# Optimization experiments

Hardware: AMD Instinct MI355X
Metric: run time of the kernel (lower is better)

## Reference

```python
import jax, jax.numpy as jnp
import numpy as np
from jax import lax

B, C, L, K = 8, 256, 4096, 65
PAD = K // 2  # torch: int(kernel.shape[-1] / 2) = 32 -> same-length output for odd K


def depthwise_corr(x, k):
    """Depthwise cross-correlation (torch conv1d semantics, no kernel flip).
    x: [B, C, L] float32, k: [K] float32 (same kernel shared by all channels,
    matching kernel.repeat(seq_len, 1)). Returns [B, C, L]."""
    w = jnp.broadcast_to(k.reshape(1, 1, K), (C, 1, K))  # [C, 1, K]
    return lax.conv_general_dilated(
        x, w, window_strides=(1,), padding=[(PAD, PAD)],
        dimension_numbers=("NCH", "OIH", "NCH"), feature_group_count=C)


def setup_inputs() -> dict:
    key = jax.random.key(0)
    k1, k2, k3 = jax.random.split(key, 3)
    return {
        "x": jax.random.normal(k1, (B, C, L), dtype=jnp.float32),
        "kernel_real": jax.random.normal(k2, (K,), dtype=jnp.float32),
        "kernel_imag": jax.random.normal(k3, (K,), dtype=jnp.float32),
        "weights_mag": jnp.ones((1, C, 1), dtype=jnp.float32),
        "weights_angle": jnp.ones((1, C, 1), dtype=jnp.float32),
    }


def reference(x, kernel_real, kernel_imag, weights_mag, weights_angle):
    # mf_coeffs = conj(kernel) -> weight = kernel_real - 1j*kernel_imag.
    # Input x is real (imag=0 after .to(complex64)), so complex conv splits
    # into two real depthwise correlations.
    yr = depthwise_corr(x, kernel_real)            # [B, C, L]
    yi = -depthwise_corr(x, kernel_imag)           # [B, C, L]
    y = lax.complex(yr, yi)                        # complex64 [B, C, L]

    # torch.std over dims (1,2), unbiased (correction=1), complex -> real std
    mean = jnp.mean(y, axis=(1, 2), keepdims=True)
    n = C * L
    var = jnp.sum(jnp.abs(y - mean) ** 2, axis=(1, 2), keepdims=True) / (n - 1)
    y = y / jnp.sqrt(var)                          # real std broadcasts over complex

    # weights_mag * y * exp(-1j * weights_angle)
    phase = lax.complex(jnp.cos(weights_angle), -jnp.sin(weights_angle))  # [1, C, 1]
    y = weights_mag * y * phase

    # FFT over the channel dim (dim=-2), then fftshift on that dim
    return jnp.fft.fftshift(jnp.fft.fft(y, axis=-2), axes=-2)
```

## Files before the change

kernel.cpp:

```cpp
#include <hip/hip_runtime.h>
#include <math.h>

#define NB 8
#define NC 256
#define NL 4096
#define NK 65

__device__ float g_stats[NB * 4];

__global__ void zero_stats_kernel() {
    if (threadIdx.x < NB * 4) g_stats[threadIdx.x] = 0.0f;
}


#define LOAD16(W, off)                                                      \
    {                                                                       \
        const int g0_ = l0 + (off);                                         \
        if (g0_ >= 0 && g0_ + 16 <= NL) {         \
            _Pragma("unroll")                                               \
            for (int q = 0; q < 4; ++q) {                                   \
                const float4 v_ = *(const float4*)(xr + g0_ + 4 * q);       \
                W[4*q+0] = v_.x; W[4*q+1] = v_.y;                           \
                W[4*q+2] = v_.z; W[4*q+3] = v_.w;                           \
            }                                                               \
        } else {                                                            \
            _Pragma("unroll")                                               \
            for (int q = 0; q < 16; ++q) {                                  \
                const int g_ = g0_ + q;                                     \
                W[q] = (g_ >= 0 && g_ < NL) ? xr[g_] : 0.0f;                \
            }                                                               \
        }                                                                   \
    }

#define CHUNK16(Lo, Hi, tb)                                                 \
    {                                                                       \
        _Pragma("unroll")                                                   \
        for (int j2 = 0; j2 < 16; ++j2) {                                   \
            const float kr_ = kre[(tb) + j2];        \
            const float ki_ = kim[(tb) + j2];                               \
            _Pragma("unroll")                                               \
            for (int i = 0; i < 16; ++i) {                                  \
                const int wi_ = i + j2;                                     \
                const float xv_ = (wi_ < 16) ? Lo[wi_] : Hi[wi_ - 16];      \
                sr[i] = fmaf(xv_, kr_, sr[i]);                              \
                si[i] = fmaf(xv_, ki_, si[i]);                              \
            }                                                               \
        }                                                                   \
    }

__global__ __launch_bounds__(256) void fused_conv_fft_kernel(
    const float* __restrict__ x,
    const float* __restrict__ kre,
    const float* __restrict__ kim,
    const float* __restrict__ wmag,
    const float* __restrict__ wang,
    float* __restrict__ out,
    int out_size)
{
    __shared__ __align__(16) float4 lbuf4[NC * 9];
    __shared__ float twr[NC], twi[NC];
    __shared__ float red[12];

    const int t = threadIdx.x;
    const int b = blockIdx.x & 7;
    const int l0 = (blockIdx.x >> 3) << 4;

    {
        float ang = (float)t * 0.024543692606170260f;
        float s, c;
        sincosf(ang, &s, &c);
        twr[t] = c; twi[t] = -s;
    }
    float sw, cw;
    sincosf(wang[t], &sw, &cw);
    const float wm = wmag[t];
    const float wgr =  wm * cw;
    const float wgi = -wm * sw;

    const float* xr = x + (size_t)b * NC * NL + (size_t)t * NL;
    const bool interleaved = (out_size >= 2 * NB * NC * NL);

    float sr[16], si[16];
    #pragma unroll
    for (int i = 0; i < 16; ++i) { sr[i] = 0.0f; si[i] = 0.0f; }

    float A[16], B[16];
    LOAD16(A, -32);
    LOAD16(B, -16);
    CHUNK16(A, B, 0);
    LOAD16(A, 0);
    CHUNK16(B, A, 16);
    LOAD16(B, 16);
    CHUNK16(A, B, 32);
    LOAD16(A, 32);
    CHUNK16(B, A, 48);
    {
        const float kr_ = kre[64];
        const float ki_ = kim[64];
        #pragma unroll
        for (int i = 0; i < 16; ++i) {
            sr[i] = fmaf(A[i], kr_, sr[i]);
            si[i] = fmaf(A[i], ki_, si[i]);
        }
    }

    float tsr = 0.0f, tsi = 0.0f, tsq = 0.0f;
    #pragma unroll
    for (int i = 0; i < 16; ++i) {
        tsr += sr[i];
        tsi -= si[i];
        tsq = fmaf(sr[i], sr[i], tsq);
        tsq = fmaf(si[i], si[i], tsq);
    }

    #pragma unroll
    for (int k = 0; k < 8; ++k) {
        float4 o;
        o.x = sr[2*k]   * wgr + si[2*k]   * wgi;
        o.y = sr[2*k]   * wgi - si[2*k]   * wgr;
        o.z = sr[2*k+1] * wgr + si[2*k+1] * wgi;
        o.w = sr[2*k+1] * wgi - si[2*k+1] * wgr;
        lbuf4[t * 9 + k] = o;
    }
    __syncthreads();

    #pragma unroll
    for (int s = 0; s < 4; ++s) {
        const int shift = 2 * s;
        const int q = 64 >> shift;
        #pragma unroll
        for (int it = 0; it < 2; ++it) {
            int task = it * 256 + t;
            int lpp = task & 7;
            int m = task >> 3;
            int j = m & (q - 1);
            int blk = m >> (6 - shift);
            int base2 = blk << (8 - shift);
            int e = j << shift;

            int ca = base2 + j;
            float4 a0 = lbuf4[ca*9 + lpp];
            float4 a1 = lbuf4[(ca + q)*9 + lpp];
            float4 a2 = lbuf4[(ca + 2*q)*9 + lpp];
            float4 a3 = lbuf4[(ca + 3*q)*9 + lpp];

            float w1r = twr[e],   w1i = twi[e];
            float w2r = twr[2*e], w2i = twi[2*e];
            float w3r = twr[3*e], w3i = twi[3*e];

            float4 b0, b1, b2, b3;
            {
                float t0r = a0.x + a2.x, t0i = a0.y + a2.y;
                float t1r = a0.x - a2.x, t1i = a0.y - a2.y;
                float t2r = a1.x + a3.x, t2i = a1.y + a3.y;
                float t3r = a1.x - a3.x, t3i = a1.y - a3.y;
                b0.x = t0r + t2r;       b0.y = t0i + t2i;
                float b2r = t0r - t2r,  b2i = t0i - t2i;
                float b1r = t1r + t3i,  b1i = t1i - t3r;
                float b3r = t1r - t3i,  b3i = t1i + t3r;
                b1.x = b1r*w1r - b1i*w1i;  b1.y = b1r*w1i + b1i*w1r;
                b2.x = b2r*w2r - b2i*w2i;  b2.y = b2r*w2i + b2i*w2r;
                b3.x = b3r*w3r - b3i*w3i;  b3.y = b3r*w3i + b3i*w3r;
            }
            {
                float t0r = a0.z + a2.z, t0i = a0.w + a2.w;
                float t1r = a0.z - a2.z, t1i = a0.w - a2.w;
                float t2r = a1.z + a3.z, t2i = a1.w + a3.w;
                float t3r = a1.z - a3.z, t3i = a1.w - a3.w;
                b0.z = t0r + t2r;       b0.w = t0i + t2i;
                float b2r = t0r - t2r,  b2i = t0i - t2i;
                float b1r = t1r + t3i,  b1i = t1i - t3r;
                float b3r = t1r - t3i,  b3i = t1i + t3r;
                b1.z = b1r*w1r - b1i*w1i;  b1.w = b1r*w1i + b1i*w1r;
                b2.z = b2r*w2r - b2i*w2i;  b2.w = b2r*w2i + b2i*w2r;
                b3.z = b3r*w3r - b3i*w3i;  b3.w = b3r*w3i + b3i*w3r;
            }
            lbuf4[ca*9 + lpp]         = b0;
            lbuf4[(ca + q)*9 + lpp]   = b1;
            lbuf4[(ca + 2*q)*9 + lpp] = b2;
            lbuf4[(ca + 3*q)*9 + lpp] = b3;
        }
        __syncthreads();
    }

    #pragma unroll
    for (int it = 0; it < 8; ++it) {
        int task = it * 256 + t;
        int lpp = task & 7;
        int pp = task >> 3;
        float4 v = lbuf4[pp*9 + lpp];
        int k = ((pp & 3) << 6) | (((pp >> 2) & 3) << 4)
              | (((pp >> 4) & 3) << 2) | ((pp >> 6) & 3);
        int cout = k ^ 128;
        if (interleaved) {
            size_t fi = 2 * ((size_t)(b * NC + cout) * NL + l0) + 4 * lpp;
            if (fi + 4 <= (size_t)out_size) *(float4*)(out + fi) = v;
        } else {
            size_t fi = (size_t)(b * NC + cout) * NL + l0 + 2 * lpp;
            if (fi + 2 <= (size_t)out_size) {
                float2 o2; o2.x = v.x; o2.y = v.z;
                *(float2*)(out + fi) = o2;
            }
        }
    }

    #pragma unroll
    for (int off = 32; off > 0; off >>= 1) {
        tsr += __shfl_down(tsr, off);
        tsi += __shfl_down(tsi, off);
        tsq += __shfl_down(tsq, off);
    }
    const int lane = t & 63, wv = t >> 6;
    if (lane == 0) { red[wv*3+0] = tsr; red[wv*3+1] = tsi; red[wv*3+2] = tsq; }
    __syncthreads();
    if (t == 0) {
        float a0 = 0.0f, a1 = 0.0f, a2 = 0.0f;
        for (int i = 0; i < 4; ++i) { a0 += red[i*3]; a1 += red[i*3+1]; a2 += red[i*3+2]; }
        atomicAdd(&g_stats[b*4+0], a0);
        atomicAdd(&g_stats[b*4+1], a1);
        atomicAdd(&g_stats[b*4+2], a2);
    }
}

__global__ __launch_bounds__(256) void scale_out_kernel(
    float* __restrict__ out, int out_size)
{
    __shared__ float sinv[NB];
    const int t = threadIdx.x;
    if (t < NB) {
        float sr = g_stats[t*4+0], si = g_stats[t*4+1], sq = g_stats[t*4+2];
        const float n = (float)(NC * NL);
        float var = (sq - (sr*sr + si*si)/n) / (n - 1.0f);
        sinv[t] = rsqrtf(var);
    }
    __syncthreads();

    const int chunk = out_size >> 3;
    const bool p2 = (chunk & (chunk - 1)) == 0;
    const int lb = 31 - __clz(chunk);
    const int n4 = out_size >> 2;
    float4* o4 = (float4*)out;
    for (int i4 = blockIdx.x * blockDim.x + t; i4 < n4;
         i4 += gridDim.x * blockDim.x) {
        int fi = i4 << 2;
        int bidx = p2 ? (fi >> lb) : (fi / chunk);
        float inv = sinv[bidx];
        float4 v = o4[i4];
        v.x *= inv; v.y *= inv; v.z *= inv; v.w *= inv;
        o4[i4] = v;
    }
    int tail0 = n4 << 2;
    int ti = tail0 + blockIdx.x * blockDim.x + t;
    if (ti < out_size) {
        int bidx = p2 ? (ti >> lb) : (ti / chunk);
        out[ti] *= sinv[bidx];
    }
}

extern "C" void kernel_launch(void* const* d_in, const int* in_sizes, int n_in,
                              void* d_out, int out_size, void* d_ws, size_t ws_size,
                              hipStream_t stream)
{
    const float* x   = (const float*)d_in[0];
    const float* kre = (const float*)d_in[1];
    const float* kim = (const float*)d_in[2];
    const float* wm  = (const float*)d_in[3];
    const float* wa  = (const float*)d_in[4];
    float* out = (float*)d_out;
    (void)d_ws; (void)ws_size;

    zero_stats_kernel<<<1, 64, 0, stream>>>();
    fused_conv_fft_kernel<<<NB * (NL / 16), 256, 0, stream>>>(x, kre, kim, wm, wa,
                                                              out, out_size);
    scale_out_kernel<<<2048, 256, 0, stream>>>(out, out_size);
}
```

Measured before the change: 151.6 us.

## Swizzle LDS layout, compute twiddles in registers, replace atomics with per-block partials

The FFT buffer moves from stride-9 padding to an XOR-swizzled layout, which cuts LDS use and allows a launch bound of 5 blocks per CU. Twiddles come from a wave shuffle of one per-lane sincos, with the higher powers derived by complex multiplication rather than read from shared tables. The global atomic statistics and the zeroing kernel are replaced by per-block partial sums that each scale block reduces itself. That block then scales its own contiguous slice, which removes a launch at the cost of redundant reductions across blocks and small twiddle rounding differences.

```diff
diff --git a/kernel.cpp b/kernel.cpp
--- a/kernel.cpp
+++ b/kernel.cpp
@@ -5,13 +5,13 @@
 #define NC 256
 #define NL 4096
 #define NK 65
-
-__device__ float g_stats[NB * 4];
-
-__global__ void zero_stats_kernel() {
-    if (threadIdx.x < NB * 4) g_stats[threadIdx.x] = 0.0f;
-}
-
+#define NSL (NL / 16)
+
+__device__ float4 g_part[NB * NSL];
+
+__device__ __forceinline__ int lidx(int row, int q) {
+    return (row << 3) + (q ^ (row & 7));
+}
 
 #define LOAD16(W, off)                                                      \
     {                                                                       \
@@ -48,7 +48,13 @@
         }                                                                   \
     }
 
-__global__ __launch_bounds__(256) void fused_conv_fft_kernel(
+__device__ __forceinline__ int digitrev_shift(int pp) {
+    int k = ((pp & 3) << 6) | (((pp >> 2) & 3) << 4)
+          | (((pp >> 4) & 3) << 2) | ((pp >> 6) & 3);
+    return k ^ 128;
+}
+
+__global__ __launch_bounds__(256, 5) void fused_conv_fft_kernel(
     const float* __restrict__ x,
     const float* __restrict__ kre,
     const float* __restrict__ kim,
@@ -57,19 +63,20 @@
     float* __restrict__ out,
     int out_size)
 {
-    __shared__ __align__(16) float4 lbuf4[NC * 9];
-    __shared__ float twr[NC], twi[NC];
-    __shared__ float red[12];
+    __shared__ __align__(16) float4 lbuf4[NC * 8];
 
     const int t = threadIdx.x;
     const int b = blockIdx.x & 7;
-    const int l0 = (blockIdx.x >> 3) << 4;
-
+    const int st = blockIdx.x >> 3;
+    const int l0 = st << 4;
+    const int lane = t & 63, wv = t >> 6;
+
+    float tw64r, tw64i;
     {
-        float ang = (float)t * 0.024543692606170260f;
+        float ang = (float)lane * 0.024543692606170260f;
         float s, c;
         sincosf(ang, &s, &c);
-        twr[t] = c; twi[t] = -s;
+        tw64r = c; tw64i = -s;
     }
     float sw, cw;
     sincosf(wang[t], &sw, &cw);
@@ -120,7 +127,7 @@
         o.y = sr[2*k]   * wgi - si[2*k]   * wgr;
         o.z = sr[2*k+1] * wgr + si[2*k+1] * wgi;
         o.w = sr[2*k+1] * wgi - si[2*k+1] * wgr;
-        lbuf4[t * 9 + k] = o;
+        lbuf4[lidx(t, k)] = o;
     }
     __syncthreads();
 
@@ -136,17 +143,25 @@
             int j = m & (q - 1);
             int blk = m >> (6 - shift);
             int base2 = blk << (8 - shift);
-            int e = j << shift;
 
             int ca = base2 + j;
-            float4 a0 = lbuf4[ca*9 + lpp];
-            float4 a1 = lbuf4[(ca + q)*9 + lpp];
-            float4 a2 = lbuf4[(ca + 2*q)*9 + lpp];
-            float4 a3 = lbuf4[(ca + 3*q)*9 + lpp];
-
-            float w1r = twr[e],   w1i = twi[e];
-            float w2r = twr[2*e], w2i = twi[2*e];
-            float w3r = twr[3*e], w3i = twi[3*e];
+            float4 a0 = lbuf4[lidx(ca, lpp)];
+            float4 a1 = lbuf4[lidx(ca + q, lpp)];
+            float4 a2 = lbuf4[lidx(ca + 2*q, lpp)];
+            float4 a3 = lbuf4[lidx(ca + 3*q, lpp)];
+
+            float w1r, w1i;
+            if (s < 3) {
+                int e = j << shift;
+                w1r = __shfl(tw64r, e);
+                w1i = __shfl(tw64i, e);
+            } else {
+                w1r = 1.0f; w1i = 0.0f;
+            }
+            float w2r = fmaf(w1r, w1r, -(w1i * w1i));
+            float w2i = 2.0f * w1r * w1i;
+            float w3r = w2r * w1r - w2i * w1i;
+            float w3i = w2r * w1i + w2i * w1r;
 
             float4 b0, b1, b2, b3;
             {
@@ -175,10 +190,10 @@
                 b2.z = b2r*w2r - b2i*w2i;  b2.w = b2r*w2i + b2i*w2r;
                 b3.z = b3r*w3r - b3i*w3i;  b3.w = b3r*w3i + b3i*w3r;
             }
-            lbuf4[ca*9 + lpp]         = b0;
-            lbuf4[(ca + q)*9 + lpp]   = b1;
-            lbuf4[(ca + 2*q)*9 + lpp] = b2;
-            lbuf4[(ca + 3*q)*9 + lpp] = b3;
+            lbuf4[lidx(ca, lpp)]         = b0;
+            lbuf4[lidx(ca + q, lpp)]     = b1;
+            lbuf4[lidx(ca + 2*q, lpp)]   = b2;
+            lbuf4[lidx(ca + 3*q, lpp)]   = b3;
         }
         __syncthreads();
     }
@@ -188,10 +203,8 @@
         int task = it * 256 + t;
         int lpp = task & 7;
         int pp = task >> 3;
-        float4 v = lbuf4[pp*9 + lpp];
-        int k = ((pp & 3) << 6) | (((pp >> 2) & 3) << 4)
-              | (((pp >> 4) & 3) << 2) | ((pp >> 6) & 3);
-        int cout = k ^ 128;
+        float4 v = lbuf4[lidx(pp, lpp)];
+        int cout = digitrev_shift(pp);
         if (interleaved) {
             size_t fi = 2 * ((size_t)(b * NC + cout) * NL + l0) + 4 * lpp;
             if (fi + 4 <= (size_t)out_size) *(float4*)(out + fi) = v;
@@ -210,50 +223,63 @@
         tsi += __shfl_down(tsi, off);
         tsq += __shfl_down(tsq, off);
     }
-    const int lane = t & 63, wv = t >> 6;
-    if (lane == 0) { red[wv*3+0] = tsr; red[wv*3+1] = tsi; red[wv*3+2] = tsq; }
+    __syncthreads();
+    float* redf = (float*)lbuf4;
+    if (lane == 0) { redf[wv*3+0] = tsr; redf[wv*3+1] = tsi; redf[wv*3+2] = tsq; }
     __syncthreads();
     if (t == 0) {
         float a0 = 0.0f, a1 = 0.0f, a2 = 0.0f;
-        for (int i = 0; i < 4; ++i) { a0 += red[i*3]; a1 += red[i*3+1]; a2 += red[i*3+2]; }
-        atomicAdd(&g_stats[b*4+0], a0);
-        atomicAdd(&g_stats[b*4+1], a1);
-        atomicAdd(&g_stats[b*4+2], a2);
+        #pragma unroll
+        for (int i = 0; i < 4; ++i) { a0 += redf[i*3]; a1 += redf[i*3+1]; a2 += redf[i*3+2]; }
+        g_part[b * NSL + st] = make_float4(a0, a1, a2, 0.0f);
     }
 }
 
 __global__ __launch_bounds__(256) void scale_out_kernel(
     float* __restrict__ out, int out_size)
 {
-    __shared__ float sinv[NB];
+    __shared__ float sred[13];
     const int t = threadIdx.x;
-    if (t < NB) {
-        float sr = g_stats[t*4+0], si = g_stats[t*4+1], sq = g_stats[t*4+2];
+    const int j = blockIdx.x;
+    const int b = j >> 8;
+    const int lane = t & 63, wv = t >> 6;
+
+    float4 p = g_part[b * NSL + t];
+    float psr = p.x, psi = p.y, psq = p.z;
+    #pragma unroll
+    for (int off = 32; off > 0; off >>= 1) {
+        psr += __shfl_down(psr, off);
+        psi += __shfl_down(psi, off);
+        psq += __shfl_down(psq, off);
+    }
+    if (lane == 0) { sred[wv*3+0] = psr; sred[wv*3+1] = psi; sred[wv*3+2] = psq; }
+    __syncthreads();
+    if (t == 0) {
+        float a0 = 0.0f, a1 = 0.0f, a2 = 0.0f;
+        #pragma unroll
+        for (int i = 0; i < 4; ++i) { a0 += sred[i*3]; a1 += sred[i*3+1]; a2 += sred[i*3+2]; }
         const float n = (float)(NC * NL);
-        float var = (sq - (sr*sr + si*si)/n) / (n - 1.0f);
-        sinv[t] = rsqrtf(var);
-    }
-    __syncthreads();
-
-    const int chunk = out_size >> 3;
-    const bool p2 = (chunk & (chunk - 1)) == 0;
-    const int lb = 31 - __clz(chunk);
-    const int n4 = out_size >> 2;
-    float4* o4 = (float4*)out;
-    for (int i4 = blockIdx.x * blockDim.x + t; i4 < n4;
-         i4 += gridDim.x * blockDim.x) {
-        int fi = i4 << 2;
-        int bidx = p2 ? (fi >> lb) : (fi / chunk);
-        float inv = sinv[bidx];
-        float4 v = o4[i4];
-        v.x *= inv; v.y *= inv; v.z *= inv; v.w *= inv;
-        o4[i4] = v;
-    }
-    int tail0 = n4 << 2;
-    int ti = tail0 + blockIdx.x * blockDim.x + t;
-    if (ti < out_size) {
-        int bidx = p2 ? (ti >> lb) : (ti / chunk);
-        out[ti] *= sinv[bidx];
+        float var = (a2 - (a0*a0 + a1*a1)/n) / (n - 1.0f);
+        sred[12] = rsqrtf(var);
+    }
+    __syncthreads();
+    const float inv = sred[12];
+
+    const int fpb = out_size >> 11;
+    const int base = j * fpb;
+    if ((fpb & 3) == 0 && ((size_t)(out + base) & 15) == 0) {
+        float4* o4 = (float4*)(out + base);
+        const int n4 = fpb >> 2;
+        for (int i = t; i < n4; i += 256) {
+            float4 v = o4[i];
+            v.x *= inv; v.y *= inv; v.z *= inv; v.w *= inv;
+            o4[i] = v;
+        }
+    } else {
+        for (int i = t; i < fpb; i += 256) out[base + i] *= inv;
+    }
+    if (j == 2047) {
+        for (int i = (fpb << 11) + t; i < out_size; i += 256) out[i] *= inv;
     }
 }
 
@@ -269,8 +295,7 @@
     float* out = (float*)d_out;
     (void)d_ws; (void)ws_size;
 
-    zero_stats_kernel<<<1, 64, 0, stream>>>();
-    fused_conv_fft_kernel<<<NB * (NL / 16), 256, 0, stream>>>(x, kre, kim, wm, wa,
-                                                              out, out_size);
+    fused_conv_fft_kernel<<<NB * NSL, 256, 0, stream>>>(x, kre, kim, wm, wa,
+                                                        out, out_size);
     scale_out_kernel<<<2048, 256, 0, stream>>>(out, out_size);
 }
```

After: 147.1 us. -2.9%, faster.
